# Kernel tuning notes

Measured on AMD Instinct MI355X. Metric: run time of the kernel, lower is better.

The kernel has to match this reference:

```python
import jax, jax.numpy as jnp
import numpy as np

B, L = 1024, 50
H = 512
N_ITEM, N_ENTITY, N_WORD = 50000, 100000, 30000


def setup_inputs() -> dict:
    key = jax.random.key(0)
    ks = jax.random.split(key, 16)
    inp = {
        "item_ids": jax.random.randint(ks[0], (B, L), 0, N_ITEM),
        "item_len": jax.random.randint(ks[1], (B,), 0, 51),
        "entity_ids": jax.random.randint(ks[2], (B, L), 0, N_ENTITY),
        "entity_len": jax.random.randint(ks[3], (B,), 0, 51),
        "word_ids": jax.random.randint(ks[4], (B, L), 0, N_WORD),
        "word_len": jax.random.randint(ks[5], (B,), 0, 51),
        "labels": jax.random.randint(ks[6], (B,), 0, N_ITEM),
        # learned parameters (torch default-ish init scales)
        "item_emb": jax.random.normal(ks[7], (N_ITEM, H), jnp.float32),
        "entity_emb": jax.random.normal(ks[8], (N_ENTITY, H), jnp.float32),
        "word_emb": jax.random.normal(ks[9], (N_WORD, H), jnp.float32),
        "W1": jax.random.normal(ks[10], (H, 4 * H), jnp.float32) / np.sqrt(H),
        "b1": jnp.zeros((4 * H,), jnp.float32),
        "W2": jax.random.normal(ks[11], (4 * H, N_ITEM), jnp.float32) / np.sqrt(4 * H),
        "b2": jnp.zeros((N_ITEM,), jnp.float32),
    }
    return inp


def _masked_mean(table, ids, lens):
    # segment-mean over ragged lists encoded as padded ids + lengths.
    # empty list -> zeros (matches the torch zero-fallback branch).
    mask = (jnp.arange(L)[None, :] < lens[:, None]).astype(table.dtype)  # [B,L]
    emb = table[ids]                                                     # [B,L,H]
    s = jnp.einsum("blh,bl->bh", emb, mask)
    denom = jnp.maximum(lens, 1).astype(table.dtype)[:, None]
    return s / denom


def reference(item_emb, entity_emb, word_emb, W1, b1, W2, b2,
              item_ids, item_len, entity_ids, entity_len,
              word_ids, word_len, labels):
    u = (_masked_mean(item_emb, item_ids, item_len)
         + _masked_mean(entity_emb, entity_ids, entity_len)
         + _masked_mean(word_emb, word_ids, word_len)) / 3.0   # [B,H]
    h = jax.nn.relu(u @ W1 + b1)                                # [B,4H]
    probs = jax.nn.softmax(h @ W2 + b2, axis=-1)                # [B,n_item]
    # faithful to source: CrossEntropyLoss applied on top of softmax outputs
    logp = jax.nn.log_softmax(probs, axis=-1)
    loss = -jnp.mean(jnp.take_along_axis(logp, labels[:, None], axis=-1))
    return probs, labels, loss
```

## Files before the change

### kernel.cpp

```cpp
#include <hip/hip_runtime.h>
#include <cstdint>
#include <cstddef>

typedef __attribute__((ext_vector_type(8))) short bf16x8;
typedef __attribute__((ext_vector_type(4))) float f32x4;

#define B_DIM 1024
#define L_SEQ 50
#define H_DIM 512
#define NITEM 50000
#define PSTRIDE 400

__device__ __forceinline__ unsigned short f2bf(float x) {
  unsigned u = __float_as_uint(x);
  return (unsigned short)((u + 0x7fffu + ((u >> 16) & 1u)) >> 16);
}
__device__ __forceinline__ unsigned pack2(float lo, float hi) {
  return (unsigned)f2bf(lo) | ((unsigned)f2bf(hi) << 16);
}
__device__ __forceinline__ void gld16(const unsigned short* g, unsigned short* l) {
  __builtin_amdgcn_global_load_lds((const __attribute__((address_space(1))) void*)g,
                                   (__attribute__((address_space(3))) void*)l, 16, 0, 0);
}
#define BAR() asm volatile("s_barrier" ::: "memory")

__global__ void mean_kernel(const int* __restrict__ item_ids, const int* __restrict__ item_len,
                            const int* __restrict__ ent_ids, const int* __restrict__ ent_len,
                            const int* __restrict__ word_ids, const int* __restrict__ word_len,
                            const float* __restrict__ item_emb, const float* __restrict__ ent_emb,
                            const float* __restrict__ word_emb, unsigned short* __restrict__ u_bf) {
  const int b = blockIdx.x >> 1;
  const int col = ((blockIdx.x & 1) << 8) + threadIdx.x;
  float out = 0.f;
  {
    const int len = item_len[b]; float a = 0.f;
#pragma unroll 4
    for (int l = 0; l < len; ++l) a += item_emb[(size_t)item_ids[b * L_SEQ + l] * H_DIM + col];
    out += a / (float)(len > 0 ? len : 1);
  }
  {
    const int len = ent_len[b]; float a = 0.f;
#pragma unroll 4
    for (int l = 0; l < len; ++l) a += ent_emb[(size_t)ent_ids[b * L_SEQ + l] * H_DIM + col];
    out += a / (float)(len > 0 ? len : 1);
  }
  {
    const int len = word_len[b]; float a = 0.f;
#pragma unroll 4
    for (int l = 0; l < len; ++l) a += word_emb[(size_t)word_ids[b * L_SEQ + l] * H_DIM + col];
    out += a / (float)(len > 0 ? len : 1);
  }
  u_bf[b * H_DIM + col] = f2bf(out / 3.f);
}

template <int K, int N>
__global__ void transpose_bf16(const float* __restrict__ W, unsigned short* __restrict__ Wt) {
  __shared__ float tile[64][65];
  const int k0 = blockIdx.x * 64, n0 = blockIdx.y * 64;
  const int tn = threadIdx.x & 63, tk = threadIdx.x >> 6;
  const int nv = (n0 + tn < N) ? n0 + tn : N - 1;
#pragma unroll
  for (int i = 0; i < 16; ++i)
    tile[tk + 4 * i][tn] = W[(size_t)(k0 + tk + 4 * i) * N + nv];
  __syncthreads();
  const int rn = threadIdx.x >> 2, ck = (threadIdx.x & 3) * 16;
  if (n0 + rn < N) {
    uint4 o[2];
    unsigned* po = (unsigned*)&o[0];
#pragma unroll
    for (int c = 0; c < 8; ++c)
      po[c] = pack2(tile[ck + 2 * c][rn], tile[ck + 2 * c + 1][rn]);
    *(uint4*)&Wt[(size_t)(n0 + rn) * K + k0 + ck] = o[0];
    *(uint4*)&Wt[(size_t)(n0 + rn) * K + k0 + ck + 8] = o[1];
  }
}

template <int K, int N, int EPI>
__global__ __launch_bounds__(512, 1) void gemm256k(const unsigned short* __restrict__ Ag,
                                                   const unsigned short* __restrict__ Btg,
                                                   const float* __restrict__ bias,
                                                   unsigned short* __restrict__ Cbf,
                                                   float* __restrict__ Cf,
                                                   float* __restrict__ pmax,
                                                   float* __restrict__ psum) {
  __shared__ unsigned short lds[8 * 8192];
  unsigned short* Aring = lds;
  unsigned short* Bring = lds + 4 * 8192;

  const int tid = threadIdx.x;
  const int lane = tid & 63;
  const int wid = tid >> 6;

  const int nwg = gridDim.x;
  const int wgid = (blockIdx.x & 7) * (nwg >> 3) + (blockIdx.x >> 3);
  const int m0 = (wgid & 3) * 256;
  const int panel = wgid >> 2;
  const int n0 = panel * 256;

  const int r0 = (wid * 2) * 16 + (lane >> 2);
  const int r1 = r0 + 16;
  const int cg = (lane & 3) ^ ((lane >> 3) & 3);
  const unsigned short* pa0 = Ag + (size_t)(m0 + r0) * K + cg * 8;
  const unsigned short* pa1 = Ag + (size_t)(m0 + r1) * K + cg * 8;
  int rg0 = n0 + r0; rg0 = rg0 < N ? rg0 : N - 1;
  int rg1 = n0 + r1; rg1 = rg1 < N ? rg1 : N - 1;
  const unsigned short* pb0 = Btg + (size_t)rg0 * K + cg * 8;
  const unsigned short* pb1 = Btg + (size_t)rg1 * K + cg * 8;
  const int li0 = wid * 2, li1 = wid * 2 + 1;

  const int wr = wid >> 2, wc = wid & 3;
  const int l15 = lane & 15, kb = lane >> 4;
  f32x4 acc[8][4] = {};

  const int HS = K / 32;
#pragma unroll
  for (int hh = 0; hh < 3; ++hh) {
    const int ko = hh * 32, sl = hh & 3;
    gld16(pa0 + ko, &Aring[sl * 8192 + li0 * 512]);
    gld16(pa1 + ko, &Aring[sl * 8192 + li1 * 512]);
    gld16(pb0 + ko, &Bring[sl * 8192 + li0 * 512]);
    gld16(pb1 + ko, &Bring[sl * 8192 + li1 * 512]);
  }
  asm volatile("s_waitcnt vmcnt(8)" ::: "memory");
  BAR();

#pragma unroll 1
  for (int h = 0; h < HS; ++h) {
    const int slot = h & 3;
    const int nslot = (h + 3) & 3;
    const int kst = (h + 3) * 32;
    const bool st = (h + 3) < HS;
    const unsigned short* As_ = &Aring[slot * 8192];
    const unsigned short* Bs_ = &Bring[slot * 8192];

    bf16x8 afA[4], bfr[4];
#pragma unroll
    for (int i = 0; i < 4; ++i) {
      const int row = wr * 128 + i * 16 + l15;
      afA[i] = *(const bf16x8*)&As_[row * 32 + (kb ^ ((row >> 1) & 3)) * 8];
    }
#pragma unroll
    for (int j = 0; j < 4; ++j) {
      const int col = wc * 64 + j * 16 + l15;
      bfr[j] = *(const bf16x8*)&Bs_[col * 32 + (kb ^ ((col >> 1) & 3)) * 8];
    }
    if (st) {
      gld16(pa0 + kst, &Aring[nslot * 8192 + li0 * 512]);
      gld16(pa1 + kst, &Aring[nslot * 8192 + li1 * 512]);
    }
    BAR();
    __builtin_amdgcn_s_setprio(1);
#pragma unroll
    for (int i = 0; i < 4; ++i)
#pragma unroll
      for (int j = 0; j < 4; ++j)
        acc[i][j] = __builtin_amdgcn_mfma_f32_16x16x32_bf16(afA[i], bfr[j], acc[i][j], 0, 0, 0);
    __builtin_amdgcn_s_setprio(0);
    BAR();

    bf16x8 afB[4];
#pragma unroll
    for (int i = 0; i < 4; ++i) {
      const int row = wr * 128 + (i + 4) * 16 + l15;
      afB[i] = *(const bf16x8*)&As_[row * 32 + (kb ^ ((row >> 1) & 3)) * 8];
    }
    if (st) {
      gld16(pb0 + kst, &Bring[nslot * 8192 + li0 * 512]);
      gld16(pb1 + kst, &Bring[nslot * 8192 + li1 * 512]);
    }
    BAR();
    __builtin_amdgcn_s_setprio(1);
#pragma unroll
    for (int i = 0; i < 4; ++i)
#pragma unroll
      for (int j = 0; j < 4; ++j)
        acc[i + 4][j] =
            __builtin_amdgcn_mfma_f32_16x16x32_bf16(afB[i], bfr[j], acc[i + 4][j], 0, 0, 0);
    __builtin_amdgcn_s_setprio(0);

    if (h + 1 < HS) {
      if (h + 4 <= HS)
        asm volatile("s_waitcnt vmcnt(8)" ::: "memory");
      else if (h + 3 == HS)
        asm volatile("s_waitcnt vmcnt(4)" ::: "memory");
      else
        asm volatile("s_waitcnt vmcnt(0)" ::: "memory");
      BAR();
    }
  }

  float bv[4];
  bool val[4];
#pragma unroll
  for (int j = 0; j < 4; ++j) {
    const int cgl = n0 + wc * 64 + 16 * j + l15;
    val[j] = (cgl < N);
    bv[j] = bias[val[j] ? cgl : 0];
  }
#pragma unroll
  for (int i = 0; i < 8; ++i) {
    const int rbase = m0 + wr * 128 + 16 * i + 4 * kb;
#pragma unroll
    for (int j = 0; j < 4; ++j) {
      if (val[j]) {
        const int cgl = n0 + wc * 64 + 16 * j + l15;
#pragma unroll
        for (int rr = 0; rr < 4; ++rr) {
          const float v = acc[i][j][rr] + bv[j];
          if (EPI == 0)
            Cbf[(size_t)(rbase + rr) * N + cgl] = f2bf(v > 0.f ? v : 0.f);
          else
            Cf[(size_t)(rbase + rr) * N + cgl] = v;
        }
      }
    }
  }

  if constexpr (EPI == 1) {
    __syncthreads();
    float* redm = (float*)&lds[0];
    float* reds = redm + 1024;
#pragma unroll
    for (int i = 0; i < 8; ++i) {
#pragma unroll
      for (int rr = 0; rr < 4; ++rr) {
        float mx = -3.0e38f;
#pragma unroll
        for (int j = 0; j < 4; ++j)
          if (val[j]) mx = fmaxf(mx, acc[i][j][rr] + bv[j]);
#pragma unroll
        for (int d = 1; d < 16; d <<= 1) mx = fmaxf(mx, __shfl_xor(mx, d));
        float s = 0.f;
#pragma unroll
        for (int j = 0; j < 4; ++j)
          if (val[j]) s += expf(acc[i][j][rr] + bv[j] - mx);
#pragma unroll
        for (int d = 1; d < 16; d <<= 1) s += __shfl_xor(s, d);
        if (l15 == 0) {
          const int rw = wr * 128 + 16 * i + 4 * kb + rr;
          redm[wc * 256 + rw] = mx;
          reds[wc * 256 + rw] = s;
        }
      }
    }
    __syncthreads();
    if (tid < 256) {
      float mm = redm[tid], ss = reds[tid];
#pragma unroll
      for (int w = 1; w < 4; ++w) {
        const float ma = redm[w * 256 + tid], sa = reds[w * 256 + tid];
        const float nm = fmaxf(mm, ma);
        ss = ss * expf(mm - nm) + sa * expf(ma - nm);
        mm = nm;
      }
      pmax[(size_t)(m0 + tid) * PSTRIDE + panel] = mm;
      psum[(size_t)(m0 + tid) * PSTRIDE + panel] = ss;
    }
  }
}

template <int K, int N, int EPI>
__global__ __launch_bounds__(256, 2) void gemm128(const unsigned short* __restrict__ Ag,
                                                  const unsigned short* __restrict__ Btg,
                                                  const float* __restrict__ bias,
                                                  unsigned short* __restrict__ Cbf,
                                                  float* __restrict__ Cf) {
  __shared__ unsigned short As[2][128 * 64];
  __shared__ unsigned short Bs[2][128 * 64];
  const int tid = threadIdx.x;
  const int lane = tid & 63;
  const int wid = tid >> 6;
  const int nwg = gridDim.x;
  const int wgid = (blockIdx.x & 7) * (nwg >> 3) + (blockIdx.x >> 3);
  const int m0 = (wgid & 7) * 128;
  const int n0 = (wgid >> 3) * 128;
  const int srsub = lane >> 3;
  const int scg = (lane & 7) ^ srsub;
  const unsigned short* pa[4];
  const unsigned short* pb[4];
#pragma unroll
  for (int qq = 0; qq < 4; ++qq) {
    const int seg = wid * 4 + qq;
    const int row = seg * 8 + srsub;
    pa[qq] = Ag + (size_t)(m0 + row) * K + scg * 8;
    int rg = n0 + row;
    rg = rg < N ? rg : N - 1;
    pb[qq] = Btg + (size_t)rg * K + scg * 8;
  }
  auto stage = [&](int t, int s) {
    const int ko = t * 64;
#pragma unroll
    for (int qq = 0; qq < 4; ++qq) {
      const int seg = wid * 4 + qq;
      gld16(pa[qq] + ko, &As[s][seg * 512]);
      gld16(pb[qq] + ko, &Bs[s][seg * 512]);
    }
  };
  const int wr = wid >> 1, wc = wid & 1;
  const int l15 = lane & 15, kb = lane >> 4;
  f32x4 acc[4][4] = {};
  auto compute = [&](int s) {
#pragma unroll
    for (int koi = 0; koi < 2; ++koi) {
      bf16x8 af[4], bf[4];
#pragma unroll
      for (int i = 0; i < 4; ++i) {
        const int row = wr * 64 + i * 16 + l15;
        af[i] = *(const bf16x8*)&As[s][row * 64 + ((koi * 4 + kb) ^ (row & 7)) * 8];
      }
#pragma unroll
      for (int j = 0; j < 4; ++j) {
        const int col = wc * 64 + j * 16 + l15;
        bf[j] = *(const bf16x8*)&Bs[s][col * 64 + ((koi * 4 + kb) ^ (col & 7)) * 8];
      }
#pragma unroll
      for (int i = 0; i < 4; ++i)
#pragma unroll
        for (int j = 0; j < 4; ++j)
          acc[i][j] = __builtin_amdgcn_mfma_f32_16x16x32_bf16(af[i], bf[j], acc[i][j], 0, 0, 0);
    }
  };
  const int NT = K / 64;
  stage(0, 0);
  asm volatile("s_waitcnt vmcnt(0)" ::: "memory");
  __syncthreads();
#pragma unroll 1
  for (int t = 0; t < NT; ++t) {
    if (t + 1 < NT) stage(t + 1, (t + 1) & 1);
    compute(t & 1);
    asm volatile("s_waitcnt vmcnt(0)" ::: "memory");
    __syncthreads();
  }
  float bv[4];
  bool val[4];
#pragma unroll
  for (int j = 0; j < 4; ++j) {
    const int cg2 = n0 + wc * 64 + 16 * j + l15;
    val[j] = (cg2 < N);
    bv[j] = bias[val[j] ? cg2 : 0];
  }
#pragma unroll
  for (int i = 0; i < 4; ++i) {
    const int rbase = m0 + wr * 64 + 16 * i + 4 * kb;
#pragma unroll
    for (int j = 0; j < 4; ++j) {
      if (val[j]) {
        const int cg2 = n0 + wc * 64 + 16 * j + l15;
#pragma unroll
        for (int rr = 0; rr < 4; ++rr) {
          const float v = acc[i][j][rr] + bv[j];
          if (EPI == 0)
            Cbf[(size_t)(rbase + rr) * N + cg2] = f2bf(v > 0.f ? v : 0.f);
          else
            Cf[(size_t)(rbase + rr) * N + cg2] = v;
        }
      }
    }
  }
}

template <int K, int N, int EPI>
__global__ __launch_bounds__(512, 2) void gemm_fused(const unsigned short* __restrict__ Ag,
                                                     const float* __restrict__ Bg,
                                                     const float* __restrict__ bias,
                                                     unsigned short* __restrict__ Cbf,
                                                     float* __restrict__ Cf,
                                                     float* __restrict__ pmax,
                                                     float* __restrict__ psum) {
  __shared__ unsigned short As[2][256 * 64];
  __shared__ uint4 Bs[2][8 * 128];
  const int tid = threadIdx.x;
  const int lane = tid & 63;
  const int wid = tid >> 6;
  const int m0 = blockIdx.x * 256;
  const int n0 = blockIdx.y * 128;
  const int arow = tid >> 3;
  const int ach = tid & 7;
  const int bn = 2 * lane;
  const int bk = 8 * wid;
  const int bcolg = (n0 + bn < N - 2) ? (n0 + bn) : (N - 2);
  uint4 areg[4];
  float2 breg[8];
  f32x4 acc[4][4] = {};
  auto stage_global = [&](int kt) {
    const int k0 = kt * 64;
#pragma unroll
    for (int qq = 0; qq < 4; ++qq)
      areg[qq] = *(const uint4*)&Ag[(size_t)(m0 + arow + 64 * qq) * K + k0 + 8 * ach];
#pragma unroll
    for (int i = 0; i < 8; ++i) breg[i] = *(const float2*)&Bg[(size_t)(k0 + bk + i) * N + bcolg];
  };
  auto stage_lds = [&](int buf) {
#pragma unroll
    for (int qq = 0; qq < 4; ++qq) {
      const int row = arow + 64 * qq;
      *(uint4*)&As[buf][row * 64 + ((8 * ach) ^ ((row & 7) * 8))] = areg[qq];
    }
    uint4 c0, c1;
    c0.x = pack2(breg[0].x, breg[1].x); c0.y = pack2(breg[2].x, breg[3].x);
    c0.z = pack2(breg[4].x, breg[5].x); c0.w = pack2(breg[6].x, breg[7].x);
    c1.x = pack2(breg[0].y, breg[1].y); c1.y = pack2(breg[2].y, breg[3].y);
    c1.z = pack2(breg[4].y, breg[5].y); c1.w = pack2(breg[6].y, breg[7].y);
    Bs[buf][wid * 128 + bn] = c0;
    Bs[buf][wid * 128 + bn + 1] = c1;
  };
  const int wr = wid & 3, wc = wid >> 2;
  const int mw = 64 * wr, nw = 64 * wc;
  const int l15 = lane & 15, kb = lane >> 4;
  auto compute = [&](int buf) {
#pragma unroll
    for (int koi = 0; koi < 2; ++koi) {
      bf16x8 af[4], bfv[4];
#pragma unroll
      for (int i = 0; i < 4; ++i) {
        const int row = mw + 16 * i + l15;
        af[i] = *(const bf16x8*)&As[buf][row * 64 + ((32 * koi + 8 * kb) ^ ((row & 7) * 8))];
      }
#pragma unroll
      for (int j = 0; j < 4; ++j)
        bfv[j] = *(const bf16x8*)&Bs[buf][(4 * koi + kb) * 128 + nw + 16 * j + l15];
#pragma unroll
      for (int i = 0; i < 4; ++i)
#pragma unroll
        for (int j = 0; j < 4; ++j)
          acc[i][j] = __builtin_amdgcn_mfma_f32_16x16x32_bf16(af[i], bfv[j], acc[i][j], 0, 0, 0);
    }
  };
  const int NT = K / 64;
  stage_global(0);
  stage_lds(0);
  __syncthreads();
  for (int t = 0; t < NT; ++t) {
    const int cur = t & 1;
    if (t + 1 < NT) stage_global(t + 1);
    compute(cur);
    if (t + 1 < NT) stage_lds(cur ^ 1);
    __syncthreads();
  }
  float bv[4];
  bool val[4];
#pragma unroll
  for (int j = 0; j < 4; ++j) {
    const int cg2 = n0 + nw + 16 * j + l15;
    val[j] = (cg2 < N);
    bv[j] = bias[val[j] ? cg2 : 0];
  }
#pragma unroll
  for (int i = 0; i < 4; ++i) {
    const int rbase = m0 + mw + 16 * i + 4 * kb;
#pragma unroll
    for (int j = 0; j < 4; ++j) {
      if (val[j]) {
        const int cg2 = n0 + nw + 16 * j + l15;
#pragma unroll
        for (int rr = 0; rr < 4; ++rr) {
          const float v = acc[i][j][rr] + bv[j];
          if (EPI == 0)
            Cbf[(size_t)(rbase + rr) * N + cg2] = f2bf(v > 0.f ? v : 0.f);
          else
            Cf[(size_t)(rbase + rr) * N + cg2] = v;
        }
      }
    }
  }
  if constexpr (EPI == 1) {
    float* redm = (float*)&As[0][0];
    float* reds = redm + 512;
#pragma unroll
    for (int i = 0; i < 4; ++i) {
#pragma unroll
      for (int rr = 0; rr < 4; ++rr) {
        float mx = -3.0e38f;
#pragma unroll
        for (int j = 0; j < 4; ++j)
          if (val[j]) mx = fmaxf(mx, acc[i][j][rr] + bv[j]);
#pragma unroll
        for (int d = 1; d < 16; d <<= 1) mx = fmaxf(mx, __shfl_xor(mx, d));
        float s = 0.f;
#pragma unroll
        for (int j = 0; j < 4; ++j)
          if (val[j]) s += expf(acc[i][j][rr] + bv[j] - mx);
#pragma unroll
        for (int d = 1; d < 16; d <<= 1) s += __shfl_xor(s, d);
        if (l15 == 0) {
          const int rl = mw + 16 * i + 4 * kb + rr;
          redm[wc * 256 + rl] = mx;
          reds[wc * 256 + rl] = s;
        }
      }
    }
    __syncthreads();
    if (tid < 256) {
      const float ma = redm[tid], mb = redm[256 + tid];
      const float mm = fmaxf(ma, mb);
      const float ss = reds[tid] * expf(ma - mm) + reds[256 + tid] * expf(mb - mm);
      pmax[(size_t)(m0 + tid) * PSTRIDE + blockIdx.y] = mm;
      psum[(size_t)(m0 + tid) * PSTRIDE + blockIdx.y] = ss;
    }
  }
}

__global__ void smax1r(const float* __restrict__ pmax, const float* __restrict__ psum,
                       float* __restrict__ rms, int ntiles) {
  const int b = blockIdx.x;
  const int l = threadIdx.x;
  float m = -3.4e38f, s = 0.f;
  for (int i = l; i < ntiles; i += 64) {
    const float pm = pmax[(size_t)b * PSTRIDE + i];
    const float ps = psum[(size_t)b * PSTRIDE + i];
    const float nm = fmaxf(m, pm);
    s = s * expf(m - nm) + ps * expf(pm - nm);
    m = nm;
  }
  for (int d = 1; d < 64; d <<= 1) {
    const float om = __shfl_xor(m, d), os = __shfl_xor(s, d);
    const float nm = fmaxf(m, om);
    s = s * expf(m - nm) + os * expf(om - nm);
    m = nm;
  }
  if (l == 0) {
    rms[b] = m;
    rms[B_DIM + b] = s;
  }
}

__global__ void smax2(float* __restrict__ buf, const float* __restrict__ rms,
                      const int* __restrict__ labels, float* __restrict__ row_lp) {
  const int b = blockIdx.x;
  float4* p = (float4*)(buf + (size_t)b * NITEM);
  const float m = rms[b];
  const float inv = 1.f / rms[B_DIM + b];
  const int lab = labels[b];
  __shared__ float s_pl;
  __shared__ float ss[256];
  float s2 = 0.f;
  for (int i = threadIdx.x; i < NITEM / 4; i += 256) {
    const float4 v = p[i];
    float pr[4];
#pragma unroll
    for (int j = 0; j < 4; ++j) {
      pr[j] = expf((&v.x)[j] - m) * inv;
      s2 += expf(pr[j] - inv);
    }
    float4 w;
    w.x = pr[0]; w.y = pr[1]; w.z = pr[2]; w.w = pr[3];
    p[i] = w;
    if ((lab >> 2) == i) s_pl = pr[lab & 3];
  }
  ss[threadIdx.x] = s2;
  __syncthreads();
  for (int off = 128; off > 0; off >>= 1) {
    if (threadIdx.x < off) ss[threadIdx.x] += ss[threadIdx.x + off];
    __syncthreads();
  }
  if (threadIdx.x == 0) row_lp[b] = s_pl - (inv + logf(ss[0]));
}

__global__ void fin(const float* __restrict__ row_lp, const int* __restrict__ labels,
                    float* __restrict__ out) {
  __shared__ float sb[256];
  float a = 0.f;
  for (int i = threadIdx.x; i < B_DIM; i += 256) {
    a += row_lp[i];
    out[(size_t)B_DIM * NITEM + i] = (float)labels[i];
  }
  sb[threadIdx.x] = a;
  __syncthreads();
  for (int off = 128; off > 0; off >>= 1) {
    if (threadIdx.x < off) sb[threadIdx.x] += sb[threadIdx.x + off];
    __syncthreads();
  }
  if (threadIdx.x == 0) out[(size_t)B_DIM * NITEM + B_DIM] = -sb[0] / (float)B_DIM;
}

extern "C" void kernel_launch(void* const* d_in, const int* in_sizes, int n_in,
                              void* d_out, int out_size, void* d_ws, size_t ws_size,
                              hipStream_t stream) {
  const int* item_ids = (const int*)d_in[0];
  const int* item_len = (const int*)d_in[1];
  const int* ent_ids = (const int*)d_in[2];
  const int* ent_len = (const int*)d_in[3];
  const int* word_ids = (const int*)d_in[4];
  const int* word_len = (const int*)d_in[5];
  const int* labels = (const int*)d_in[6];
  const float* item_emb = (const float*)d_in[7];
  const float* ent_emb = (const float*)d_in[8];
  const float* word_emb = (const float*)d_in[9];
  const float* W1 = (const float*)d_in[10];
  const float* b1 = (const float*)d_in[11];
  const float* W2 = (const float*)d_in[12];
  const float* b2 = (const float*)d_in[13];

  float* out = (float*)d_out;
  char* ws = (char*)d_ws;
  unsigned short* u_bf = (unsigned short*)ws;
  unsigned short* h_bf = (unsigned short*)(ws + (1 << 20));
  float* pmax = (float*)(ws + 5 * (1 << 20));
  float* psum = (float*)(ws + 7 * (1 << 20));
  float* rms = (float*)(ws + 9 * (1 << 20));
  float* row_lp = rms + 2 * B_DIM;
  unsigned short* W1t = (unsigned short*)(ws + 10 * (1 << 20));
  unsigned short* W2t = (unsigned short*)(ws + 16 * (1 << 20));
  float* logits = out;

  const size_t need = (size_t)16 * (1 << 20) + (size_t)NITEM * 2048 * 2;
  const bool fast = ws_size >= need;

  mean_kernel<<<2 * B_DIM, 256, 0, stream>>>(item_ids, item_len, ent_ids, ent_len, word_ids,
                                             word_len, item_emb, ent_emb, word_emb, u_bf);
  if (fast) {
    transpose_bf16<512, 2048><<<dim3(8, 32), 256, 0, stream>>>(W1, W1t);
    transpose_bf16<2048, NITEM><<<dim3(32, 782), 256, 0, stream>>>(W2, W2t);
    gemm128<512, 2048, 0><<<8 * 16, 256, 0, stream>>>(u_bf, W1t, b1, h_bf, nullptr);
    gemm256k<2048, NITEM, 1><<<4 * 196, 512, 0, stream>>>(h_bf, W2t, b2, nullptr, logits, pmax,
                                                          psum);
    smax1r<<<B_DIM, 64, 0, stream>>>(pmax, psum, rms, 196);
  } else {
    gemm_fused<512, 2048, 0><<<dim3(4, 16), 512, 0, stream>>>(u_bf, W1, b1, h_bf, nullptr,
                                                              nullptr, nullptr);
    gemm_fused<2048, NITEM, 1><<<dim3(4, 391), 512, 0, stream>>>(h_bf, W2, b2, nullptr, logits,
                                                                 pmax, psum);
    smax1r<<<B_DIM, 64, 0, stream>>>(pmax, psum, rms, 391);
  }
  smax2<<<B_DIM, 256, 0, stream>>>(logits, rms, labels, row_lp);
  fin<<<1, 256, 0, stream>>>(row_lp, labels, out);
}
```

Measured before the change: 585.9 us.

## Shrink W2 GEMM tile to 128x256 and fuse mean/transpose launches

Replaces the 256x256 output-tile GEMM for the big vocab projection with a 128x256 tile using one barrier per k-step and half the accumulators, doubling the workgroup count to 1568. It also merges the mean-pooling kernel and both weight transposes into a single prep kernel to remove launch gaps. The smaller tile raises occupancy and balances work across CUs, but halves A/B reuse per tile, so more B traffic goes to L2/HBM. The single barrier per step with loads issued earlier may also change how memory overlaps with MFMA.

```diff
diff --git a/kernel.cpp b/kernel.cpp
--- a/kernel.cpp
+++ b/kernel.cpp
@@ -24,13 +24,18 @@
 }
 #define BAR() asm volatile("s_barrier" ::: "memory")
 
-__global__ void mean_kernel(const int* __restrict__ item_ids, const int* __restrict__ item_len,
-                            const int* __restrict__ ent_ids, const int* __restrict__ ent_len,
-                            const int* __restrict__ word_ids, const int* __restrict__ word_len,
-                            const float* __restrict__ item_emb, const float* __restrict__ ent_emb,
-                            const float* __restrict__ word_emb, unsigned short* __restrict__ u_bf) {
-  const int b = blockIdx.x >> 1;
-  const int col = ((blockIdx.x & 1) << 8) + threadIdx.x;
+__device__ __forceinline__ void mean_body(int b2, const int* __restrict__ item_ids,
+                                          const int* __restrict__ item_len,
+                                          const int* __restrict__ ent_ids,
+                                          const int* __restrict__ ent_len,
+                                          const int* __restrict__ word_ids,
+                                          const int* __restrict__ word_len,
+                                          const float* __restrict__ item_emb,
+                                          const float* __restrict__ ent_emb,
+                                          const float* __restrict__ word_emb,
+                                          unsigned short* __restrict__ u_bf) {
+  const int b = b2 >> 1;
+  const int col = ((b2 & 1) << 8) + threadIdx.x;
   float out = 0.f;
   {
     const int len = item_len[b]; float a = 0.f;
@@ -53,10 +58,18 @@
   u_bf[b * H_DIM + col] = f2bf(out / 3.f);
 }
 
-template <int K, int N>
-__global__ void transpose_bf16(const float* __restrict__ W, unsigned short* __restrict__ Wt) {
-  __shared__ float tile[64][65];
-  const int k0 = blockIdx.x * 64, n0 = blockIdx.y * 64;
+__global__ void mean_kernel(const int* __restrict__ item_ids, const int* __restrict__ item_len,
+                            const int* __restrict__ ent_ids, const int* __restrict__ ent_len,
+                            const int* __restrict__ word_ids, const int* __restrict__ word_len,
+                            const float* __restrict__ item_emb, const float* __restrict__ ent_emb,
+                            const float* __restrict__ word_emb, unsigned short* __restrict__ u_bf) {
+  mean_body(blockIdx.x, item_ids, item_len, ent_ids, ent_len, word_ids, word_len, item_emb,
+            ent_emb, word_emb, u_bf);
+}
+
+__device__ __forceinline__ void transpose_body(const float* __restrict__ W,
+                                               unsigned short* __restrict__ Wt, int K, int N,
+                                               int k0, int n0, float (*tile)[65]) {
   const int tn = threadIdx.x & 63, tk = threadIdx.x >> 6;
   const int nv = (n0 + tn < N) ? n0 + tn : N - 1;
 #pragma unroll
@@ -75,17 +88,44 @@
   }
 }
 
+__global__ void prep_kernel(const int* __restrict__ item_ids, const int* __restrict__ item_len,
+                            const int* __restrict__ ent_ids, const int* __restrict__ ent_len,
+                            const int* __restrict__ word_ids, const int* __restrict__ word_len,
+                            const float* __restrict__ item_emb, const float* __restrict__ ent_emb,
+                            const float* __restrict__ word_emb, unsigned short* __restrict__ u_bf,
+                            const float* __restrict__ W1, unsigned short* __restrict__ W1t,
+                            const float* __restrict__ W2, unsigned short* __restrict__ W2t) {
+  __shared__ float tile[64][65];
+  const int b = blockIdx.x;
+  if (b < 2048) {
+    mean_body(b, item_ids, item_len, ent_ids, ent_len, word_ids, word_len, item_emb, ent_emb,
+              word_emb, u_bf);
+  } else if (b < 2048 + 25024) {
+    const int t = b - 2048;
+    transpose_body(W2, W2t, 2048, NITEM, (t & 31) * 64, (t >> 5) * 64, tile);
+  } else {
+    const int t = b - (2048 + 25024);
+    transpose_body(W1, W1t, 512, 2048, (t & 7) * 64, (t >> 3) * 64, tile);
+  }
+}
+
+template <int K, int N>
+__global__ void transpose_bf16(const float* __restrict__ W, unsigned short* __restrict__ Wt) {
+  __shared__ float tile[64][65];
+  transpose_body(W, Wt, K, N, blockIdx.x * 64, blockIdx.y * 64, tile);
+}
+
 template <int K, int N, int EPI>
-__global__ __launch_bounds__(512, 1) void gemm256k(const unsigned short* __restrict__ Ag,
-                                                   const unsigned short* __restrict__ Btg,
-                                                   const float* __restrict__ bias,
-                                                   unsigned short* __restrict__ Cbf,
-                                                   float* __restrict__ Cf,
-                                                   float* __restrict__ pmax,
-                                                   float* __restrict__ psum) {
-  __shared__ unsigned short lds[8 * 8192];
+__global__ __launch_bounds__(512, 1) void gemm128x256(const unsigned short* __restrict__ Ag,
+                                                      const unsigned short* __restrict__ Btg,
+                                                      const float* __restrict__ bias,
+                                                      unsigned short* __restrict__ Cbf,
+                                                      float* __restrict__ Cf,
+                                                      float* __restrict__ pmax,
+                                                      float* __restrict__ psum) {
+  __shared__ unsigned short lds[4 * 4096 + 4 * 8192];
   unsigned short* Aring = lds;
-  unsigned short* Bring = lds + 4 * 8192;
+  unsigned short* Bring = lds + 4 * 4096;
 
   const int tid = threadIdx.x;
   const int lane = tid & 63;
@@ -93,35 +133,33 @@
 
   const int nwg = gridDim.x;
   const int wgid = (blockIdx.x & 7) * (nwg >> 3) + (blockIdx.x >> 3);
-  const int m0 = (wgid & 3) * 256;
-  const int panel = wgid >> 2;
+  const int m0 = (wgid & 7) * 128;
+  const int panel = wgid >> 3;
   const int n0 = panel * 256;
 
-  const int r0 = (wid * 2) * 16 + (lane >> 2);
-  const int r1 = r0 + 16;
   const int cg = (lane & 3) ^ ((lane >> 3) & 3);
-  const unsigned short* pa0 = Ag + (size_t)(m0 + r0) * K + cg * 8;
-  const unsigned short* pa1 = Ag + (size_t)(m0 + r1) * K + cg * 8;
-  int rg0 = n0 + r0; rg0 = rg0 < N ? rg0 : N - 1;
-  int rg1 = n0 + r1; rg1 = rg1 < N ? rg1 : N - 1;
+  const int arow = wid * 16 + (lane >> 2);
+  const unsigned short* pa = Ag + (size_t)(m0 + arow) * K + cg * 8;
+  const int br0 = wid * 32 + (lane >> 2), br1 = br0 + 16;
+  int rg0 = n0 + br0; rg0 = rg0 < N ? rg0 : N - 1;
+  int rg1 = n0 + br1; rg1 = rg1 < N ? rg1 : N - 1;
   const unsigned short* pb0 = Btg + (size_t)rg0 * K + cg * 8;
   const unsigned short* pb1 = Btg + (size_t)rg1 * K + cg * 8;
   const int li0 = wid * 2, li1 = wid * 2 + 1;
 
   const int wr = wid >> 2, wc = wid & 3;
   const int l15 = lane & 15, kb = lane >> 4;
-  f32x4 acc[8][4] = {};
+  f32x4 acc[4][4] = {};
 
   const int HS = K / 32;
 #pragma unroll
   for (int hh = 0; hh < 3; ++hh) {
-    const int ko = hh * 32, sl = hh & 3;
-    gld16(pa0 + ko, &Aring[sl * 8192 + li0 * 512]);
-    gld16(pa1 + ko, &Aring[sl * 8192 + li1 * 512]);
-    gld16(pb0 + ko, &Bring[sl * 8192 + li0 * 512]);
-    gld16(pb1 + ko, &Bring[sl * 8192 + li1 * 512]);
-  }
-  asm volatile("s_waitcnt vmcnt(8)" ::: "memory");
+    const int ko = hh * 32;
+    gld16(pa + ko, &Aring[hh * 4096 + wid * 512]);
+    gld16(pb0 + ko, &Bring[hh * 8192 + li0 * 512]);
+    gld16(pb1 + ko, &Bring[hh * 8192 + li1 * 512]);
+  }
+  asm volatile("s_waitcnt vmcnt(6)" ::: "memory");
   BAR();
 
 #pragma unroll 1
@@ -129,60 +167,39 @@
     const int slot = h & 3;
     const int nslot = (h + 3) & 3;
     const int kst = (h + 3) * 32;
-    const bool st = (h + 3) < HS;
-    const unsigned short* As_ = &Aring[slot * 8192];
+    const unsigned short* As_ = &Aring[slot * 4096];
     const unsigned short* Bs_ = &Bring[slot * 8192];
 
-    bf16x8 afA[4], bfr[4];
+    if (h + 3 < HS) {
+      gld16(pa + kst, &Aring[nslot * 4096 + wid * 512]);
+      gld16(pb0 + kst, &Bring[nslot * 8192 + li0 * 512]);
+      gld16(pb1 + kst, &Bring[nslot * 8192 + li1 * 512]);
+    }
+
+    bf16x8 af[4], bf[4];
 #pragma unroll
     for (int i = 0; i < 4; ++i) {
-      const int row = wr * 128 + i * 16 + l15;
-      afA[i] = *(const bf16x8*)&As_[row * 32 + (kb ^ ((row >> 1) & 3)) * 8];
+      const int row = wr * 64 + i * 16 + l15;
+      af[i] = *(const bf16x8*)&As_[row * 32 + (kb ^ ((row >> 1) & 3)) * 8];
     }
 #pragma unroll
     for (int j = 0; j < 4; ++j) {
       const int col = wc * 64 + j * 16 + l15;
-      bfr[j] = *(const bf16x8*)&Bs_[col * 32 + (kb ^ ((col >> 1) & 3)) * 8];
-    }
-    if (st) {
-      gld16(pa0 + kst, &Aring[nslot * 8192 + li0 * 512]);
-      gld16(pa1 + kst, &Aring[nslot * 8192 + li1 * 512]);
-    }
-    BAR();
+      bf[j] = *(const bf16x8*)&Bs_[col * 32 + (kb ^ ((col >> 1) & 3)) * 8];
+    }
     __builtin_amdgcn_s_setprio(1);
 #pragma unroll
     for (int i = 0; i < 4; ++i)
 #pragma unroll
       for (int j = 0; j < 4; ++j)
-        acc[i][j] = __builtin_amdgcn_mfma_f32_16x16x32_bf16(afA[i], bfr[j], acc[i][j], 0, 0, 0);
-    __builtin_amdgcn_s_setprio(0);
-    BAR();
-
-    bf16x8 afB[4];
-#pragma unroll
-    for (int i = 0; i < 4; ++i) {
-      const int row = wr * 128 + (i + 4) * 16 + l15;
-      afB[i] = *(const bf16x8*)&As_[row * 32 + (kb ^ ((row >> 1) & 3)) * 8];
-    }
-    if (st) {
-      gld16(pb0 + kst, &Bring[nslot * 8192 + li0 * 512]);
-      gld16(pb1 + kst, &Bring[nslot * 8192 + li1 * 512]);
-    }
-    BAR();
-    __builtin_amdgcn_s_setprio(1);
-#pragma unroll
-    for (int i = 0; i < 4; ++i)
-#pragma unroll
-      for (int j = 0; j < 4; ++j)
-        acc[i + 4][j] =
-            __builtin_amdgcn_mfma_f32_16x16x32_bf16(afB[i], bfr[j], acc[i + 4][j], 0, 0, 0);
+        acc[i][j] = __builtin_amdgcn_mfma_f32_16x16x32_bf16(af[i], bf[j], acc[i][j], 0, 0, 0);
     __builtin_amdgcn_s_setprio(0);
 
     if (h + 1 < HS) {
       if (h + 4 <= HS)
-        asm volatile("s_waitcnt vmcnt(8)" ::: "memory");
+        asm volatile("s_waitcnt vmcnt(6)" ::: "memory");
       else if (h + 3 == HS)
-        asm volatile("s_waitcnt vmcnt(4)" ::: "memory");
+        asm volatile("s_waitcnt vmcnt(3)" ::: "memory");
       else
         asm volatile("s_waitcnt vmcnt(0)" ::: "memory");
       BAR();
@@ -198,8 +215,8 @@
     bv[j] = bias[val[j] ? cgl : 0];
   }
 #pragma unroll
-  for (int i = 0; i < 8; ++i) {
-    const int rbase = m0 + wr * 128 + 16 * i + 4 * kb;
+  for (int i = 0; i < 4; ++i) {
+    const int rbase = m0 + wr * 64 + 16 * i + 4 * kb;
 #pragma unroll
     for (int j = 0; j < 4; ++j) {
       if (val[j]) {
@@ -219,9 +236,9 @@
   if constexpr (EPI == 1) {
     __syncthreads();
     float* redm = (float*)&lds[0];
-    float* reds = redm + 1024;
-#pragma unroll
-    for (int i = 0; i < 8; ++i) {
+    float* reds = redm + 512;
+#pragma unroll
+    for (int i = 0; i < 4; ++i) {
 #pragma unroll
       for (int rr = 0; rr < 4; ++rr) {
         float mx = -3.0e38f;
@@ -237,18 +254,18 @@
 #pragma unroll
         for (int d = 1; d < 16; d <<= 1) s += __shfl_xor(s, d);
         if (l15 == 0) {
-          const int rw = wr * 128 + 16 * i + 4 * kb + rr;
-          redm[wc * 256 + rw] = mx;
-          reds[wc * 256 + rw] = s;
+          const int rw = wr * 64 + 16 * i + 4 * kb + rr;
+          redm[wc * 128 + rw] = mx;
+          reds[wc * 128 + rw] = s;
         }
       }
     }
     __syncthreads();
-    if (tid < 256) {
+    if (tid < 128) {
       float mm = redm[tid], ss = reds[tid];
 #pragma unroll
       for (int w = 1; w < 4; ++w) {
-        const float ma = redm[w * 256 + tid], sa = reds[w * 256 + tid];
+        const float ma = redm[w * 128 + tid], sa = reds[w * 128 + tid];
         const float nm = fmaxf(mm, ma);
         ss = ss * expf(mm - nm) + sa * expf(ma - nm);
         mm = nm;
@@ -606,16 +623,17 @@
   const size_t need = (size_t)16 * (1 << 20) + (size_t)NITEM * 2048 * 2;
   const bool fast = ws_size >= need;
 
-  mean_kernel<<<2 * B_DIM, 256, 0, stream>>>(item_ids, item_len, ent_ids, ent_len, word_ids,
-                                             word_len, item_emb, ent_emb, word_emb, u_bf);
   if (fast) {
-    transpose_bf16<512, 2048><<<dim3(8, 32), 256, 0, stream>>>(W1, W1t);
-    transpose_bf16<2048, NITEM><<<dim3(32, 782), 256, 0, stream>>>(W2, W2t);
+    prep_kernel<<<2048 + 25024 + 256, 256, 0, stream>>>(item_ids, item_len, ent_ids, ent_len,
+                                                        word_ids, word_len, item_emb, ent_emb,
+                                                        word_emb, u_bf, W1, W1t, W2, W2t);
     gemm128<512, 2048, 0><<<8 * 16, 256, 0, stream>>>(u_bf, W1t, b1, h_bf, nullptr);
-    gemm256k<2048, NITEM, 1><<<4 * 196, 512, 0, stream>>>(h_bf, W2t, b2, nullptr, logits, pmax,
-                                                          psum);
+    gemm128x256<2048, NITEM, 1><<<8 * 196, 512, 0, stream>>>(h_bf, W2t, b2, nullptr, logits,
+                                                             pmax, psum);
     smax1r<<<B_DIM, 64, 0, stream>>>(pmax, psum, rms, 196);
   } else {
+    mean_kernel<<<2 * B_DIM, 256, 0, stream>>>(item_ids, item_len, ent_ids, ent_len, word_ids,
+                                               word_len, item_emb, ent_emb, word_emb, u_bf);
     gemm_fused<512, 2048, 0><<<dim3(4, 16), 512, 0, stream>>>(u_bf, W1, b1, h_bf, nullptr,
                                                               nullptr, nullptr);
     gemm_fused<2048, NITEM, 1><<<dim3(4, 391), 512, 0, stream>>>(h_bf, W2, b2, nullptr, logits,
```

Result: slower. 618.8 us (+5.6%).
